# Kernel optimization log

Hardware: AMD Instinct MI355X
Metric: run time of the kernel (lower is better)

The kernel has to match this reference:

```python
import jax, jax.numpy as jnp
import numpy as np

HIDDEN = 1024
H = 16        # num query heads
HKV = 4       # num kv heads
GROUPS = H // HKV
D = HIDDEN // H  # head_dim = 64
SW = (63, 0)  # sliding_window (left, right)
W = SW[0] + SW[1] + 1  # window length per query = 64
MAXPOS = 2048


def _sincos_table(num_pos, dim):
    # faithful to create_sinusoidal_positions (incl. final [:, :, :num_pos] slice)
    inv_freq = 1.0 / 10000 ** (np.arange(0, dim, 2, dtype=np.int32) / dim)
    freqs = np.einsum('i,j->ij', np.arange(num_pos, dtype=np.int32), inv_freq).astype(np.float32)
    emb = np.concatenate((freqs, freqs), axis=-1)
    out = np.concatenate((np.sin(emb)[:, None, :], np.cos(emb)[:, None, :]), axis=-1)
    return jnp.asarray(out[:, :, :num_pos])  # [num_pos, 1, 2*dim]

_SINCOS = _sincos_table(MAXPOS, D)


def _rotate_half(x):
    h = x.shape[-1] // 2
    return jnp.concatenate((-x[..., h:], x[..., :h]), axis=-1)


def setup_inputs() -> dict:
    key = jax.random.key(0)
    k0, k1, k2, k3, k4 = jax.random.split(key, 5)
    B, S = 1, 2048
    std = 0.02
    return {
        'hidden_states': jax.random.normal(k0, (B, S, HIDDEN), dtype=jnp.float32),
        'attention_mask': jnp.ones((B, S, 1, W), dtype=jnp.int32),
        'position_ids': jnp.arange(B * S, dtype=jnp.int32).reshape(B, S) % MAXPOS,
        'q_kernel': jax.random.normal(k1, (HIDDEN, H * D), dtype=jnp.float32) * std,
        'k_kernel': jax.random.normal(k2, (HIDDEN, HKV * D), dtype=jnp.float32) * std,
        'v_kernel': jax.random.normal(k3, (HIDDEN, HKV * D), dtype=jnp.float32) * std,
        'o_kernel': jax.random.normal(k4, (HIDDEN, HIDDEN), dtype=jnp.float32) * std,
    }


def reference(hidden_states, attention_mask, position_ids, q_kernel, k_kernel, v_kernel, o_kernel):
    B, S, _ = hidden_states.shape
    # QKV projections (no bias)
    q = (hidden_states @ q_kernel).reshape(B, S, H, D)
    k = (hidden_states @ k_kernel).reshape(B, S, HKV, D)
    v = (hidden_states @ v_kernel).reshape(B, S, HKV, D)
    # rotary embedding; sincos[pos] -> [B,S,1,2D], broadcasts over head axis
    sc = _SINCOS[position_ids]
    sin, cos = jnp.split(sc, 2, axis=-1)
    k = k * cos + _rotate_half(k) * sin
    q = q * cos + _rotate_half(q) * sin
    # GQA: repeat kv heads to match query heads
    k = jnp.repeat(k, GROUPS, axis=2)  # [B,S,H,D]
    v = jnp.repeat(v, GROUPS, axis=2)
    # sliding-window gather: each query position sees W surrounding keys
    k = jnp.pad(k, ((0, 0), SW, (0, 0), (0, 0)))
    v = jnp.pad(v, ((0, 0), SW, (0, 0), (0, 0)))
    idx = jnp.arange(W, dtype=jnp.int32)[None, :] + jnp.arange(S, dtype=jnp.int32)[:, None]  # [S,W]
    kg = k[:, idx]  # [B,S,W,H,D]
    vg = v[:, idx]
    # attention (q_len=1 per position), scores [B,S,H,W]
    scores = jnp.einsum('bshd,bswhd->bshw', q, kg) / jnp.asarray(np.sqrt(D), scores_dtype := jnp.float32)
    neg = jnp.finfo(jnp.float32).min
    m = attention_mask[:, :, 0, :][:, :, None, :]  # [B,S,1,W] broadcast over H
    bias = jnp.where(m > 0, jnp.float32(0.0), neg)
    weights = jax.nn.softmax(scores + bias, axis=-1)
    attn = jnp.einsum('bshw,bswhd->bshd', weights, vg).reshape(B, S, HIDDEN)
    return attn @ o_kernel
```

## Files before the change

### kernel.cpp

```cpp
#include <hip/hip_runtime.h>
#include <hip/hip_bf16.h>
#include <math.h>

#define S        2048
#define HIDDEN   1024
#define NH       16
#define NKV      4
#define HD       64
#define NQKV     1536

typedef _Float16 f16x8 __attribute__((ext_vector_type(8)));
typedef _Float16 f16x4 __attribute__((ext_vector_type(4)));
typedef float    f32x4 __attribute__((ext_vector_type(4)));

__global__ __launch_bounds__(256) void prep_kernel(const float* __restrict__ wq, const float* __restrict__ wk,
                                                   const float* __restrict__ wvv, const float* __restrict__ wo,
                                                   _Float16* __restrict__ wqkvT, _Float16* __restrict__ woT) {
    int bid = blockIdx.x;
    int tid = threadIdx.x;
    const float* src; _Float16* dst; int Cn, b;
    if (bid < 1024)      { src = wq;  dst = wqkvT;                       Cn = 1024; b = bid; }
    else if (bid < 1280) { src = wk;  dst = wqkvT + (size_t)1024 * 1024; Cn = 256;  b = bid - 1024; }
    else if (bid < 1536) { src = wvv; dst = wqkvT + (size_t)1280 * 1024; Cn = 256;  b = bid - 1280; }
    else                 { src = wo;  dst = woT;                         Cn = 1024; b = bid - 1536; }
    int xb = Cn >> 5;
    int c0 = (b % xb) * 32;
    int r0 = (b / xb) * 32;
    __shared__ float t[32][33];
    int tx = tid & 31, ty = tid >> 5;
#pragma unroll
    for (int i = ty; i < 32; i += 8)
        t[i][tx] = src[(size_t)(r0 + i) * Cn + c0 + tx];
    __syncthreads();
#pragma unroll
    for (int i = ty; i < 32; i += 8)
        dst[(size_t)(c0 + i) * 1024 + r0 + tx] = (_Float16)t[tx][i];
}

template <bool F32A, typename OutT>
__global__ __launch_bounds__(256) void gemm_pipe(const void* __restrict__ Avoid,
                                                 const _Float16* __restrict__ BT,
                                                 OutT* __restrict__ C,
                                                 int M, int N, int K) {
    const float*    Af = (const float*)Avoid;
    const _Float16* Ah = (const _Float16*)Avoid;
    const int m0   = blockIdx.y * 128;
    const int n0   = blockIdx.x * 64;
    const int tid  = threadIdx.x;
    const int lane = tid & 63;
    const int wv   = tid >> 6;
    const int lr   = lane & 15;
    const int quad = lane >> 4;
    const int wm   = (wv >> 1) * 64;
    const int wn   = (wv & 1) * 32;

    __shared__ __align__(16) _Float16 As[2][128 * 64];
    __shared__ __align__(16) _Float16 Bs[2][64 * 64];

    const int ar8 = tid >> 3, ac8 = tid & 7;
    const int ar4 = tid >> 4, ac4 = tid & 15;

    f32x4 acc[4][2] = {};
    float4 aRf[8];
    uint4  aRh[4];
    uint4  bR[2];

    if (F32A) {
#pragma unroll
        for (int i = 0; i < 8; ++i) {
            int r = ar4 + i * 16;
            float4 v = *(const float4*)(Af + (size_t)(m0 + r) * K + ac4 * 4);
            f16x4 h = { (_Float16)v.x, (_Float16)v.y, (_Float16)v.z, (_Float16)v.w };
            *(f16x4*)&As[0][r * 64 + ac4 * 4] = h;
        }
    } else {
#pragma unroll
        for (int i = 0; i < 4; ++i) {
            int r = ar8 + i * 32;
            *(uint4*)&As[0][r * 64 + ac8 * 8] = *(const uint4*)(Ah + (size_t)(m0 + r) * K + ac8 * 8);
        }
    }
#pragma unroll
    for (int i = 0; i < 2; ++i) {
        int r = ar8 + i * 32;
        *(uint4*)&Bs[0][r * 64 + ac8 * 8] = *(const uint4*)(BT + (size_t)(n0 + r) * K + ac8 * 8);
    }
    __syncthreads();

    int p = 0;
    for (int k0 = 64; k0 < K; k0 += 64) {
        if (F32A) {
#pragma unroll
            for (int i = 0; i < 8; ++i)
                aRf[i] = *(const float4*)(Af + (size_t)(m0 + ar4 + i * 16) * K + k0 + ac4 * 4);
        } else {
#pragma unroll
            for (int i = 0; i < 4; ++i)
                aRh[i] = *(const uint4*)(Ah + (size_t)(m0 + ar8 + i * 32) * K + k0 + ac8 * 8);
        }
#pragma unroll
        for (int i = 0; i < 2; ++i)
            bR[i] = *(const uint4*)(BT + (size_t)(n0 + ar8 + i * 32) * K + k0 + ac8 * 8);

#pragma unroll
        for (int ks = 0; ks < 2; ++ks) {
            f16x8 a[4], b[2];
#pragma unroll
            for (int i = 0; i < 4; ++i)
                a[i] = *(const f16x8*)&As[p][(wm + i * 16 + lr) * 64 + (ks * 4 + quad) * 8];
#pragma unroll
            for (int j = 0; j < 2; ++j)
                b[j] = *(const f16x8*)&Bs[p][(wn + j * 16 + lr) * 64 + (ks * 4 + quad) * 8];
#pragma unroll
            for (int i = 0; i < 4; ++i)
#pragma unroll
                for (int j = 0; j < 2; ++j)
                    acc[i][j] = __builtin_amdgcn_mfma_f32_16x16x32_f16(a[i], b[j], acc[i][j], 0, 0, 0);
        }

        if (F32A) {
#pragma unroll
            for (int i = 0; i < 8; ++i) {
                float4 v = aRf[i];
                f16x4 h = { (_Float16)v.x, (_Float16)v.y, (_Float16)v.z, (_Float16)v.w };
                *(f16x4*)&As[p ^ 1][(ar4 + i * 16) * 64 + ac4 * 4] = h;
            }
        } else {
#pragma unroll
            for (int i = 0; i < 4; ++i)
                *(uint4*)&As[p ^ 1][(ar8 + i * 32) * 64 + ac8 * 8] = aRh[i];
        }
#pragma unroll
        for (int i = 0; i < 2; ++i)
            *(uint4*)&Bs[p ^ 1][(ar8 + i * 32) * 64 + ac8 * 8] = bR[i];
        __syncthreads();
        p ^= 1;
    }

#pragma unroll
    for (int ks = 0; ks < 2; ++ks) {
        f16x8 a[4], b[2];
#pragma unroll
        for (int i = 0; i < 4; ++i)
            a[i] = *(const f16x8*)&As[p][(wm + i * 16 + lr) * 64 + (ks * 4 + quad) * 8];
#pragma unroll
        for (int j = 0; j < 2; ++j)
            b[j] = *(const f16x8*)&Bs[p][(wn + j * 16 + lr) * 64 + (ks * 4 + quad) * 8];
#pragma unroll
        for (int i = 0; i < 4; ++i)
#pragma unroll
            for (int j = 0; j < 2; ++j)
                acc[i][j] = __builtin_amdgcn_mfma_f32_16x16x32_f16(a[i], b[j], acc[i][j], 0, 0, 0);
    }

#pragma unroll
    for (int i = 0; i < 4; ++i)
#pragma unroll
        for (int j = 0; j < 2; ++j)
#pragma unroll
            for (int r = 0; r < 4; ++r)
                C[(size_t)(m0 + wm + i * 16 + quad * 4 + r) * N + n0 + wn + j * 16 + lr] = (OutT)acc[i][j][r];
}

__global__ __launch_bounds__(256) void attn_mfma(const _Float16* __restrict__ qkv,
                                                 const int* __restrict__ mask,
                                                 const int* __restrict__ pos_ids,
                                                 _Float16* __restrict__ attn_out) {
    const int s0   = blockIdx.x * 16;
    const int g    = blockIdx.y;
    const int tid  = threadIdx.x;
    const int lane = tid & 63;
    const int wv   = tid >> 6;
    const int h    = g * 4 + wv;
    const int lr   = lane & 15;
    const int quad = lane >> 4;

    __shared__ __align__(16) _Float16 K_lds[80 * 72];
    __shared__ __align__(16) _Float16 Vt_lds[64 * 104];
    __shared__ __align__(16) _Float16 P_lds[4][16 * 104];
    __shared__ int M_lds[1024];
    __shared__ double invf[32];

    ((int4*)M_lds)[tid] = ((const int4*)(mask + s0 * 64))[tid];
    if (tid < 32) invf[tid] = pow(10000.0, -(double)(2 * tid) / 64.0);
    __syncthreads();

    for (int c = tid; c < 320; c += 256) {
        int r = c >> 2, cl = c & 3;
        int j = s0 - 63 + r;
        f16x8 nlo = {}, nhi = {};
        if (j >= 0 && r < 79) {
            f16x8 lo = *(const f16x8*)(qkv + (size_t)j * NQKV + 1024 + g * 64 + cl * 8);
            f16x8 hi = *(const f16x8*)(qkv + (size_t)j * NQKV + 1024 + g * 64 + 32 + cl * 8);
            int pos = pos_ids[j];
#pragma unroll
            for (int e = 0; e < 8; ++e) {
                float ang = (float)((double)pos * invf[cl * 8 + e]);
                float sn, cs;
                sincosf(ang, &sn, &cs);
                float x1 = (float)lo[e], x2 = (float)hi[e];
                nlo[e] = (_Float16)(x1 * cs - x2 * sn);
                nhi[e] = (_Float16)(x2 * cs + x1 * sn);
            }
        }
        *(f16x8*)&K_lds[r * 72 + cl * 8]       = nlo;
        *(f16x8*)&K_lds[r * 72 + (cl + 4) * 8] = nhi;
    }
    for (int c = tid; c < 96 * 8; c += 256) {
        int r = c >> 3, cl = c & 7;
        int j = s0 - 63 + r;
        f16x8 val = {};
        if (j >= 0 && r < 79)
            val = *(const f16x8*)(qkv + (size_t)j * NQKV + 1280 + g * 64 + cl * 8);
#pragma unroll
        for (int d8 = 0; d8 < 8; ++d8)
            Vt_lds[(cl * 8 + d8) * 104 + r] = val[d8];
    }

    f16x8 qf[2];
    {
        int posq = pos_ids[s0 + lr];
        f16x8 q0 = *(const f16x8*)(qkv + (size_t)(s0 + lr) * NQKV + h * 64 + quad * 8);
        f16x8 q1 = *(const f16x8*)(qkv + (size_t)(s0 + lr) * NQKV + h * 64 + 32 + quad * 8);
        f16x8 n0, n1;
#pragma unroll
        for (int e = 0; e < 8; ++e) {
            float ang = (float)((double)posq * invf[quad * 8 + e]);
            float sn, cs;
            sincosf(ang, &sn, &cs);
            float x1 = (float)q0[e], x2 = (float)q1[e];
            n0[e] = (_Float16)((x1 * cs - x2 * sn) * 0.125f);
            n1[e] = (_Float16)((x2 * cs + x1 * sn) * 0.125f);
        }
        qf[0] = n0; qf[1] = n1;
    }
    __syncthreads();

    f32x4 sc[5];
#pragma unroll
    for (int t = 0; t < 5; ++t) {
        f32x4 a = {};
#pragma unroll
        for (int ks = 0; ks < 2; ++ks) {
            f16x8 kf = *(const f16x8*)&K_lds[(t * 16 + lr) * 72 + ks * 32 + quad * 8];
            a = __builtin_amdgcn_mfma_f32_16x16x32_f16(qf[ks], kf, a, 0, 0, 0);
        }
        sc[t] = a;
    }

#pragma unroll
    for (int t = 0; t < 5; ++t)
#pragma unroll
        for (int r = 0; r < 4; ++r) {
            int qi = quad * 4 + r;
            int w  = t * 16 + lr - qi;
            bool ok = (w >= 0) && (w < 64) && (M_lds[qi * 64 + (w & 63)] > 0);
            sc[t][r] = ok ? sc[t][r] : -1e30f;
        }

    float pr[5][4];
#pragma unroll
    for (int r = 0; r < 4; ++r) {
        float mx = -1e30f;
#pragma unroll
        for (int t = 0; t < 5; ++t) mx = fmaxf(mx, sc[t][r]);
#pragma unroll
        for (int off = 1; off < 16; off <<= 1) mx = fmaxf(mx, __shfl_xor(mx, off));
        float sum = 0.f;
#pragma unroll
        for (int t = 0; t < 5; ++t) { float e = __expf(sc[t][r] - mx); pr[t][r] = e; sum += e; }
#pragma unroll
        for (int off = 1; off < 16; off <<= 1) sum += __shfl_xor(sum, off);
        float rs = 1.0f / sum;
#pragma unroll
        for (int t = 0; t < 5; ++t) pr[t][r] *= rs;
    }

    _Float16* myP = P_lds[wv];
    {
        f16x4 z = {};
        *(f16x4*)&myP[lr * 104 + 80 + quad * 4] = z;
    }
#pragma unroll
    for (int t = 0; t < 5; ++t)
#pragma unroll
        for (int r = 0; r < 4; ++r)
            myP[(quad * 4 + r) * 104 + t * 16 + lr] = (_Float16)pr[t][r];
    __syncthreads();

    f32x4 oacc[4] = {};
#pragma unroll
    for (int ks = 0; ks < 3; ++ks) {
        f16x8 pf = *(const f16x8*)&myP[lr * 104 + ks * 32 + quad * 8];
#pragma unroll
        for (int t = 0; t < 4; ++t) {
            f16x8 vf = *(const f16x8*)&Vt_lds[(t * 16 + lr) * 104 + ks * 32 + quad * 8];
            oacc[t] = __builtin_amdgcn_mfma_f32_16x16x32_f16(pf, vf, oacc[t], 0, 0, 0);
        }
    }
#pragma unroll
    for (int t = 0; t < 4; ++t)
#pragma unroll
        for (int r = 0; r < 4; ++r)
            attn_out[(size_t)(s0 + quad * 4 + r) * HIDDEN + h * 64 + t * 16 + lr] = (_Float16)oacc[t][r];
}

extern "C" void kernel_launch(void* const* d_in, const int* in_sizes, int n_in,
                              void* d_out, int out_size, void* d_ws, size_t ws_size,
                              hipStream_t stream) {
    const float* hs      = (const float*)d_in[0];
    const int*   mask    = (const int*)  d_in[1];
    const int*   pos_ids = (const int*)  d_in[2];
    const float* wq      = (const float*)d_in[3];
    const float* wk      = (const float*)d_in[4];
    const float* wvv     = (const float*)d_in[5];
    const float* wo      = (const float*)d_in[6];
    float* out = (float*)d_out;

    char* ws = (char*)d_ws;
    _Float16* wqkvT   = (_Float16*)(ws + 0);
    _Float16* woT     = (_Float16*)(ws + (3u << 20));
    _Float16* qkvf16  = (_Float16*)(ws + (5u << 20));
    _Float16* attnf16 = (_Float16*)(ws + (11u << 20));

    prep_kernel<<<2560, 256, 0, stream>>>(wq, wk, wvv, wo, wqkvT, woT);
    gemm_pipe<true, _Float16><<<dim3(NQKV / 64, S / 128), 256, 0, stream>>>(hs, wqkvT, qkvf16, S, NQKV, HIDDEN);
    attn_mfma<<<dim3(S / 16, NKV), 256, 0, stream>>>(qkvf16, mask, pos_ids, attnf16);
    gemm_pipe<false, float><<<dim3(HIDDEN / 64, S / 128), 256, 0, stream>>>(attnf16, woT, out, S, HIDDEN, HIDDEN);
}
```

Baseline: 128.4 us.

## Fuse RoPE into QKV GEMM epilogue, pre-transpose V, convert activations once

Applies rotary embedding and the query scale in the QKV GEMM epilogue, using a sin/cos table built in the prep kernel. This removes per-block sincos recomputation and the redundant K rotation in attention. V is written transposed and padded by the GEMM so attention loads it with vector copies instead of a scalar transpose, and hidden states are converted to fp16 once in prep. LDS rows are padded to 72 to avoid bank conflicts. The cost is extra prep work and workspace traffic, plus a more complex epilogue with scattered stores.

```diff
diff --git a/kernel.cpp b/kernel.cpp
--- a/kernel.cpp
+++ b/kernel.cpp
@@ -8,16 +8,42 @@
 #define NKV      4
 #define HD       64
 #define NQKV     1536
+#define VW       2128
 
 typedef _Float16 f16x8 __attribute__((ext_vector_type(8)));
 typedef _Float16 f16x4 __attribute__((ext_vector_type(4)));
 typedef float    f32x4 __attribute__((ext_vector_type(4)));
 
-__global__ __launch_bounds__(256) void prep_kernel(const float* __restrict__ wq, const float* __restrict__ wk,
+__global__ __launch_bounds__(256) void prep_kernel(const float* __restrict__ hs, _Float16* __restrict__ hsf16,
+                                                   const float* __restrict__ wq, const float* __restrict__ wk,
                                                    const float* __restrict__ wvv, const float* __restrict__ wo,
-                                                   _Float16* __restrict__ wqkvT, _Float16* __restrict__ woT) {
+                                                   _Float16* __restrict__ wqkvT, _Float16* __restrict__ woT,
+                                                   const int* __restrict__ pos_ids, float2* __restrict__ rope_tab,
+                                                   _Float16* __restrict__ vTs) {
     int bid = blockIdx.x;
     int tid = threadIdx.x;
+    if (bid >= 4864) {
+        int d = bid - 4864;
+        if (tid < 64) vTs[(size_t)d * VW + tid] = (_Float16)0.0f;
+        return;
+    }
+    if (bid >= 4608) {
+        int idx = (bid - 4608) * 256 + tid;
+        int s = idx >> 5, f = idx & 31;
+        double inv = pow(10000.0, -(double)(2 * f) / 64.0);
+        float ang = (float)((double)pos_ids[s] * inv);
+        float sn, cs;
+        sincosf(ang, &sn, &cs);
+        rope_tab[idx] = make_float2(sn, cs);
+        return;
+    }
+    if (bid >= 2560) {
+        int i = (bid - 2560) * 256 + tid;
+        float4 v = ((const float4*)hs)[i];
+        f16x4 o = { (_Float16)v.x, (_Float16)v.y, (_Float16)v.z, (_Float16)v.w };
+        *(f16x4*)(hsf16 + 4 * (size_t)i) = o;
+        return;
+    }
     const float* src; _Float16* dst; int Cn, b;
     if (bid < 1024)      { src = wq;  dst = wqkvT;                       Cn = 1024; b = bid; }
     else if (bid < 1280) { src = wk;  dst = wqkvT + (size_t)1024 * 1024; Cn = 256;  b = bid - 1024; }
@@ -37,13 +63,121 @@
         dst[(size_t)(c0 + i) * 1024 + r0 + tx] = (_Float16)t[tx][i];
 }
 
-template <bool F32A, typename OutT>
-__global__ __launch_bounds__(256) void gemm_pipe(const void* __restrict__ Avoid,
-                                                 const _Float16* __restrict__ BT,
-                                                 OutT* __restrict__ C,
-                                                 int M, int N, int K) {
-    const float*    Af = (const float*)Avoid;
-    const _Float16* Ah = (const _Float16*)Avoid;
+__global__ __launch_bounds__(256) void gemm_qkv(const _Float16* __restrict__ A,
+                                                const _Float16* __restrict__ BT,
+                                                _Float16* __restrict__ qkv,
+                                                _Float16* __restrict__ vTs,
+                                                const float2* __restrict__ rope_tab) {
+    const int K = HIDDEN;
+    const int m0   = blockIdx.y * 128;
+    const int n0   = blockIdx.x * 64;
+    const int tid  = threadIdx.x;
+    const int lane = tid & 63;
+    const int wv   = tid >> 6;
+    const int lr   = lane & 15;
+    const int quad = lane >> 4;
+    const int wm   = wv * 32;
+
+    __shared__ __align__(16) _Float16 As[2][128 * 72];
+    __shared__ __align__(16) _Float16 Bs[2][64 * 72];
+
+    const int ar8 = tid >> 3, ac8 = tid & 7;
+
+    f32x4 acc[2][4] = {};
+    uint4 aR[4], bR[2];
+
+#pragma unroll
+    for (int i = 0; i < 4; ++i)
+        *(uint4*)&As[0][(ar8 + i * 32) * 72 + ac8 * 8] = *(const uint4*)(A + (size_t)(m0 + ar8 + i * 32) * K + ac8 * 8);
+#pragma unroll
+    for (int i = 0; i < 2; ++i)
+        *(uint4*)&Bs[0][(ar8 + i * 32) * 72 + ac8 * 8] = *(const uint4*)(BT + (size_t)(n0 + ar8 + i * 32) * K + ac8 * 8);
+    __syncthreads();
+
+    int p = 0;
+    for (int k0 = 64; k0 < K; k0 += 64) {
+#pragma unroll
+        for (int i = 0; i < 4; ++i)
+            aR[i] = *(const uint4*)(A + (size_t)(m0 + ar8 + i * 32) * K + k0 + ac8 * 8);
+#pragma unroll
+        for (int i = 0; i < 2; ++i)
+            bR[i] = *(const uint4*)(BT + (size_t)(n0 + ar8 + i * 32) * K + k0 + ac8 * 8);
+#pragma unroll
+        for (int ks = 0; ks < 2; ++ks) {
+            f16x8 a[2], b[4];
+#pragma unroll
+            for (int i = 0; i < 2; ++i)
+                a[i] = *(const f16x8*)&As[p][(wm + i * 16 + lr) * 72 + (ks * 4 + quad) * 8];
+#pragma unroll
+            for (int j = 0; j < 4; ++j)
+                b[j] = *(const f16x8*)&Bs[p][(j * 16 + lr) * 72 + (ks * 4 + quad) * 8];
+#pragma unroll
+            for (int i = 0; i < 2; ++i)
+#pragma unroll
+                for (int j = 0; j < 4; ++j)
+                    acc[i][j] = __builtin_amdgcn_mfma_f32_16x16x32_f16(a[i], b[j], acc[i][j], 0, 0, 0);
+        }
+#pragma unroll
+        for (int i = 0; i < 4; ++i)
+            *(uint4*)&As[p ^ 1][(ar8 + i * 32) * 72 + ac8 * 8] = aR[i];
+#pragma unroll
+        for (int i = 0; i < 2; ++i)
+            *(uint4*)&Bs[p ^ 1][(ar8 + i * 32) * 72 + ac8 * 8] = bR[i];
+        __syncthreads();
+        p ^= 1;
+    }
+#pragma unroll
+    for (int ks = 0; ks < 2; ++ks) {
+        f16x8 a[2], b[4];
+#pragma unroll
+        for (int i = 0; i < 2; ++i)
+            a[i] = *(const f16x8*)&As[p][(wm + i * 16 + lr) * 72 + (ks * 4 + quad) * 8];
+#pragma unroll
+        for (int j = 0; j < 4; ++j)
+            b[j] = *(const f16x8*)&Bs[p][(j * 16 + lr) * 72 + (ks * 4 + quad) * 8];
+#pragma unroll
+        for (int i = 0; i < 2; ++i)
+#pragma unroll
+            for (int j = 0; j < 4; ++j)
+                acc[i][j] = __builtin_amdgcn_mfma_f32_16x16x32_f16(a[i], b[j], acc[i][j], 0, 0, 0);
+    }
+
+    if (n0 < 1280) {
+        const bool isq = (n0 < 1024);
+#pragma unroll
+        for (int i = 0; i < 2; ++i)
+#pragma unroll
+            for (int r = 0; r < 4; ++r) {
+                int s = m0 + wm + i * 16 + quad * 4 + r;
+                const float2* tb = rope_tab + (size_t)s * 32;
+#pragma unroll
+                for (int j = 0; j < 2; ++j) {
+                    float2 sc = tb[j * 16 + lr];
+                    float lo = acc[i][j][r], hi = acc[i][j + 2][r];
+                    float nlo = lo * sc.y - hi * sc.x;
+                    float nhi = hi * sc.y + lo * sc.x;
+                    if (isq) { nlo *= 0.125f; nhi *= 0.125f; }
+                    qkv[(size_t)s * NQKV + n0 + j * 16 + lr]      = (_Float16)nlo;
+                    qkv[(size_t)s * NQKV + n0 + 32 + j * 16 + lr] = (_Float16)nhi;
+                }
+            }
+    } else {
+#pragma unroll
+        for (int i = 0; i < 2; ++i)
+#pragma unroll
+            for (int j = 0; j < 4; ++j) {
+                int d = n0 - 1280 + j * 16 + lr;
+                f16x4 h = { (_Float16)acc[i][j][0], (_Float16)acc[i][j][1],
+                            (_Float16)acc[i][j][2], (_Float16)acc[i][j][3] };
+                *(f16x4*)(vTs + (size_t)d * VW + 64 + m0 + wm + i * 16 + quad * 4) = h;
+            }
+    }
+}
+
+__global__ __launch_bounds__(256) void gemm_o(const _Float16* __restrict__ A,
+                                              const _Float16* __restrict__ BT,
+                                              float* __restrict__ C) {
+    const int K = HIDDEN, N = HIDDEN;
     const int m0   = blockIdx.y * 128;
     const int n0   = blockIdx.x * 64;
     const int tid  = threadIdx.x;
@@ -54,117 +188,80 @@
     const int wm   = (wv >> 1) * 64;
     const int wn   = (wv & 1) * 32;
 
-    __shared__ __align__(16) _Float16 As[2][128 * 64];
-    __shared__ __align__(16) _Float16 Bs[2][64 * 64];
+    __shared__ __align__(16) _Float16 As[2][128 * 72];
+    __shared__ __align__(16) _Float16 Bs[2][64 * 72];
 
     const int ar8 = tid >> 3, ac8 = tid & 7;
-    const int ar4 = tid >> 4, ac4 = tid & 15;
-
     f32x4 acc[4][2] = {};
-    float4 aRf[8];
-    uint4  aRh[4];
-    uint4  bR[2];
-
-    if (F32A) {
-#pragma unroll
-        for (int i = 0; i < 8; ++i) {
-            int r = ar4 + i * 16;
-            float4 v = *(const float4*)(Af + (size_t)(m0 + r) * K + ac4 * 4);
-            f16x4 h = { (_Float16)v.x, (_Float16)v.y, (_Float16)v.z, (_Float16)v.w };
-            *(f16x4*)&As[0][r * 64 + ac4 * 4] = h;
-        }
-    } else {
-#pragma unroll
-        for (int i = 0; i < 4; ++i) {
-            int r = ar8 + i * 32;
-            *(uint4*)&As[0][r * 64 + ac8 * 8] = *(const uint4*)(Ah + (size_t)(m0 + r) * K + ac8 * 8);
-        }
-    }
-#pragma unroll
-    for (int i = 0; i < 2; ++i) {
-        int r = ar8 + i * 32;
-        *(uint4*)&Bs[0][r * 64 + ac8 * 8] = *(const uint4*)(BT + (size_t)(n0 + r) * K + ac8 * 8);
-    }
+    uint4 aR[4], bR[2];
+
+#pragma unroll
+    for (int i = 0; i < 4; ++i)
+        *(uint4*)&As[0][(ar8 + i * 32) * 72 + ac8 * 8] = *(const uint4*)(A + (size_t)(m0 + ar8 + i * 32) * K + ac8 * 8);
+#pragma unroll
+    for (int i = 0; i < 2; ++i)
+        *(uint4*)&Bs[0][(ar8 + i * 32) * 72 + ac8 * 8] = *(const uint4*)(BT + (size_t)(n0 + ar8 + i * 32) * K + ac8 * 8);
     __syncthreads();
 
     int p = 0;
     for (int k0 = 64; k0 < K; k0 += 64) {
-        if (F32A) {
-#pragma unroll
-            for (int i = 0; i < 8; ++i)
-                aRf[i] = *(const float4*)(Af + (size_t)(m0 + ar4 + i * 16) * K + k0 + ac4 * 4);
-        } else {
-#pragma unroll
-            for (int i = 0; i < 4; ++i)
-                aRh[i] = *(const uint4*)(Ah + (size_t)(m0 + ar8 + i * 32) * K + k0 + ac8 * 8);
-        }
+#pragma unroll
+        for (int i = 0; i < 4; ++i)
+            aR[i] = *(const uint4*)(A + (size_t)(m0 + ar8 + i * 32) * K + k0 + ac8 * 8);
 #pragma unroll
         for (int i = 0; i < 2; ++i)
             bR[i] = *(const uint4*)(BT + (size_t)(n0 + ar8 + i * 32) * K + k0 + ac8 * 8);
-
 #pragma unroll
         for (int ks = 0; ks < 2; ++ks) {
             f16x8 a[4], b[2];
 #pragma unroll
             for (int i = 0; i < 4; ++i)
-                a[i] = *(const f16x8*)&As[p][(wm + i * 16 + lr) * 64 + (ks * 4 + quad) * 8];
+                a[i] = *(const f16x8*)&As[p][(wm + i * 16 + lr) * 72 + (ks * 4 + quad) * 8];
 #pragma unroll
             for (int j = 0; j < 2; ++j)
-                b[j] = *(const f16x8*)&Bs[p][(wn + j * 16 + lr) * 64 + (ks * 4 + quad) * 8];
+                b[j] = *(const f16x8*)&Bs[p][(wn + j * 16 + lr) * 72 + (ks * 4 + quad) * 8];
 #pragma unroll
             for (int i = 0; i < 4; ++i)
 #pragma unroll
                 for (int j = 0; j < 2; ++j)
                     acc[i][j] = __builtin_amdgcn_mfma_f32_16x16x32_f16(a[i], b[j], acc[i][j], 0, 0, 0);
         }
-
-        if (F32A) {
-#pragma unroll
-            for (int i = 0; i < 8; ++i) {
-                float4 v = aRf[i];
-                f16x4 h = { (_Float16)v.x, (_Float16)v.y, (_Float16)v.z, (_Float16)v.w };
-                *(f16x4*)&As[p ^ 1][(ar4 + i * 16) * 64 + ac4 * 4] = h;
-            }
-        } else {
-#pragma unroll
-            for (int i = 0; i < 4; ++i)
-                *(uint4*)&As[p ^ 1][(ar8 + i * 32) * 64 + ac8 * 8] = aRh[i];
-        }
-#pragma unroll
-        for (int i = 0; i < 2; ++i)
-            *(uint4*)&Bs[p ^ 1][(ar8 + i * 32) * 64 + ac8 * 8] = bR[i];
+#pragma unroll
+        for (int i = 0; i < 4; ++i)
+            *(uint4*)&As[p ^ 1][(ar8 + i * 32) * 72 + ac8 * 8] = aR[i];
+#pragma unroll
+        for (int i = 0; i < 2; ++i)
+            *(uint4*)&Bs[p ^ 1][(ar8 + i * 32) * 72 + ac8 * 8] = bR[i];
         __syncthreads();
         p ^= 1;
     }
-
 #pragma unroll
     for (int ks = 0; ks < 2; ++ks) {
         f16x8 a[4], b[2];
 #pragma unroll
         for (int i = 0; i < 4; ++i)
-            a[i] = *(const f16x8*)&As[p][(wm + i * 16 + lr) * 64 + (ks * 4 + quad) * 8];
+            a[i] = *(const f16x8*)&As[p][(wm + i * 16 + lr) * 72 + (ks * 4 + quad) * 8];
 #pragma unroll
         for (int j = 0; j < 2; ++j)
-            b[j] = *(const f16x8*)&Bs[p][(wn + j * 16 + lr) * 64 + (ks * 4 + quad) * 8];
+            b[j] = *(const f16x8*)&Bs[p][(wn + j * 16 + lr) * 72 + (ks * 4 + quad) * 8];
 #pragma unroll
         for (int i = 0; i < 4; ++i)
 #pragma unroll
             for (int j = 0; j < 2; ++j)
                 acc[i][j] = __builtin_amdgcn_mfma_f32_16x16x32_f16(a[i], b[j], acc[i][j], 0, 0, 0);
     }
-
 #pragma unroll
     for (int i = 0; i < 4; ++i)
 #pragma unroll
         for (int j = 0; j < 2; ++j)
 #pragma unroll
             for (int r = 0; r < 4; ++r)
-                C[(size_t)(m0 + wm + i * 16 + quad * 4 + r) * N + n0 + wn + j * 16 + lr] = (OutT)acc[i][j][r];
+                C[(size_t)(m0 + wm + i * 16 + quad * 4 + r) * N + n0 + wn + j * 16 + lr] = acc[i][j][r];
 }
 
 __global__ __launch_bounds__(256) void attn_mfma(const _Float16* __restrict__ qkv,
+                                                 const _Float16* __restrict__ vTs,
                                                  const int* __restrict__ mask,
-                                                 const int* __restrict__ pos_ids,
                                                  _Float16* __restrict__ attn_out) {
     const int s0   = blockIdx.x * 16;
     const int g    = blockIdx.y;
@@ -179,61 +276,27 @@
     __shared__ __align__(16) _Float16 Vt_lds[64 * 104];
     __shared__ __align__(16) _Float16 P_lds[4][16 * 104];
     __shared__ int M_lds[1024];
-    __shared__ double invf[32];
 
     ((int4*)M_lds)[tid] = ((const int4*)(mask + s0 * 64))[tid];
-    if (tid < 32) invf[tid] = pow(10000.0, -(double)(2 * tid) / 64.0);
-    __syncthreads();
-
-    for (int c = tid; c < 320; c += 256) {
-        int r = c >> 2, cl = c & 3;
-        int j = s0 - 63 + r;
-        f16x8 nlo = {}, nhi = {};
-        if (j >= 0 && r < 79) {
-            f16x8 lo = *(const f16x8*)(qkv + (size_t)j * NQKV + 1024 + g * 64 + cl * 8);
-            f16x8 hi = *(const f16x8*)(qkv + (size_t)j * NQKV + 1024 + g * 64 + 32 + cl * 8);
-            int pos = pos_ids[j];
-#pragma unroll
-            for (int e = 0; e < 8; ++e) {
-                float ang = (float)((double)pos * invf[cl * 8 + e]);
-                float sn, cs;
-                sincosf(ang, &sn, &cs);
-                float x1 = (float)lo[e], x2 = (float)hi[e];
-                nlo[e] = (_Float16)(x1 * cs - x2 * sn);
-                nhi[e] = (_Float16)(x2 * cs + x1 * sn);
-            }
-        }
-        *(f16x8*)&K_lds[r * 72 + cl * 8]       = nlo;
-        *(f16x8*)&K_lds[r * 72 + (cl + 4) * 8] = nhi;
-    }
-    for (int c = tid; c < 96 * 8; c += 256) {
-        int r = c >> 3, cl = c & 7;
-        int j = s0 - 63 + r;
+
+    for (int c = tid; c < 640; c += 256) {
+        int r = c >> 3, cc = c & 7;
+        int j = s0 - 64 + r;
         f16x8 val = {};
-        if (j >= 0 && r < 79)
-            val = *(const f16x8*)(qkv + (size_t)j * NQKV + 1280 + g * 64 + cl * 8);
-#pragma unroll
-        for (int d8 = 0; d8 < 8; ++d8)
-            Vt_lds[(cl * 8 + d8) * 104 + r] = val[d8];
+        if (j >= 0)
+            val = *(const f16x8*)(qkv + (size_t)j * NQKV + 1024 + g * 64 + cc * 8);
+        *(f16x8*)&K_lds[r * 72 + cc * 8] = val;
+    }
+    for (int c = tid; c < 64 * 12; c += 256) {
+        int d = c / 12, ch = c % 12;
+        *(f16x8*)&Vt_lds[d * 104 + ch * 8] =
+            *(const f16x8*)(vTs + (size_t)(g * 64 + d) * VW + s0 + ch * 8);
     }
 
     f16x8 qf[2];
-    {
-        int posq = pos_ids[s0 + lr];
-        f16x8 q0 = *(const f16x8*)(qkv + (size_t)(s0 + lr) * NQKV + h * 64 + quad * 8);
-        f16x8 q1 = *(const f16x8*)(qkv + (size_t)(s0 + lr) * NQKV + h * 64 + 32 + quad * 8);
-        f16x8 n0, n1;
-#pragma unroll
-        for (int e = 0; e < 8; ++e) {
-            float ang = (float)((double)posq * invf[quad * 8 + e]);
-            float sn, cs;
-            sincosf(ang, &sn, &cs);
-            float x1 = (float)q0[e], x2 = (float)q1[e];
-            n0[e] = (_Float16)((x1 * cs - x2 * sn) * 0.125f);
-            n1[e] = (_Float16)((x2 * cs + x1 * sn) * 0.125f);
-        }
-        qf[0] = n0; qf[1] = n1;
-    }
+#pragma unroll
+    for (int ks = 0; ks < 2; ++ks)
+        qf[ks] = *(const f16x8*)(qkv + (size_t)(s0 + lr) * NQKV + h * 64 + ks * 32 + quad * 8);
     __syncthreads();
 
     f32x4 sc[5];
@@ -253,7 +316,7 @@
 #pragma unroll
         for (int r = 0; r < 4; ++r) {
             int qi = quad * 4 + r;
-            int w  = t * 16 + lr - qi;
+            int w  = t * 16 + lr - 1 - qi;
             bool ok = (w >= 0) && (w < 64) && (M_lds[qi * 64 + (w & 63)] > 0);
             sc[t][r] = ok ? sc[t][r] : -1e30f;
         }
@@ -320,11 +383,15 @@
     char* ws = (char*)d_ws;
     _Float16* wqkvT   = (_Float16*)(ws + 0);
     _Float16* woT     = (_Float16*)(ws + (3u << 20));
-    _Float16* qkvf16  = (_Float16*)(ws + (5u << 20));
-    _Float16* attnf16 = (_Float16*)(ws + (11u << 20));
-
-    prep_kernel<<<2560, 256, 0, stream>>>(wq, wk, wvv, wo, wqkvT, woT);
-    gemm_pipe<true, _Float16><<<dim3(NQKV / 64, S / 128), 256, 0, stream>>>(hs, wqkvT, qkvf16, S, NQKV, HIDDEN);
-    attn_mfma<<<dim3(S / 16, NKV), 256, 0, stream>>>(qkvf16, mask, pos_ids, attnf16);
-    gemm_pipe<false, float><<<dim3(HIDDEN / 64, S / 128), 256, 0, stream>>>(attnf16, woT, out, S, HIDDEN, HIDDEN);
-}
+    _Float16* hsf16   = (_Float16*)(ws + (5u << 20));
+    _Float16* qkvf16  = (_Float16*)(ws + (9u << 20));
+    _Float16* attnf16 = (_Float16*)(ws + (15u << 20));
+    _Float16* vTs     = (_Float16*)(ws + (19u << 20));
+    float2*   ropeTab = (float2*)  (ws + (21u << 20));
+
+    prep_kernel<<<5120, 256, 0, stream>>>(hs, hsf16, wq, wk, wvv, wo, wqkvT, woT,
+                                          pos_ids, ropeTab, vTs);
+    gemm_qkv<<<dim3(NQKV / 64, S / 128), 256, 0, stream>>>(hsf16, wqkvT, qkvf16, vTs, ropeTab);
+    attn_mfma<<<dim3(S / 16, NKV), 256, 0, stream>>>(qkvf16, vTs, mask, attnf16);
+    gemm_o<<<dim3(HIDDEN / 64, S / 128), 256, 0, stream>>>(attnf16, woT, out);
+}
```

New measurement: 119.0 us. 7.3% less time.
